# Performance work log

Hardware: AMD Instinct MI355X
Metric: run time of the kernel (lower is better)

## Reference

```python
import jax, jax.numpy as jnp
import numpy as np

HEADS = 16
DIM_HEAD = 64
SCALE = DIM_HEAD ** -0.5
EPS = 1e-5


def layer_norm(x, gamma):
    mu = jnp.mean(x, axis=-1, keepdims=True)
    var = jnp.var(x, axis=-1, keepdims=True)
    return (x - mu) * jax.lax.rsqrt(var + EPS) * gamma


def setup_inputs() -> dict:
    key = jax.random.key(0)
    ks = jax.random.split(key, 5)
    B, S, D = 2, 2048, 1024
    x = jax.random.normal(ks[0], (B, S, D), dtype=jnp.float32)
    gamma = jnp.ones((D,), dtype=jnp.float32)
    Wq = jax.random.normal(ks[1], (D, HEADS * DIM_HEAD), dtype=jnp.float32) * (D ** -0.5)
    Wkv = jax.random.normal(ks[2], (D, 2 * DIM_HEAD), dtype=jnp.float32) * (D ** -0.5)
    Wo = jax.random.normal(ks[3], (HEADS * DIM_HEAD, D), dtype=jnp.float32) * ((HEADS * DIM_HEAD) ** -0.5)
    return {"x": x, "gamma": gamma, "Wq": Wq, "Wkv": Wkv, "Wo": Wo}


def reference(x, gamma, Wq, Wkv, Wo):
    B, S, D = x.shape
    kv_input = x  # context=None -> self attention
    xn = layer_norm(x, gamma)
    q = xn @ Wq                          # [B,S,H*Dh]
    kv = kv_input @ Wkv                  # [B,S,2*Dh]
    k, v = jnp.split(kv, 2, axis=-1)     # each [B,S,Dh]
    q = q.reshape(B, S, HEADS, DIM_HEAD).transpose(0, 2, 1, 3) * SCALE  # [B,H,S,Dh]
    sim = jnp.einsum('bhid,bjd->bhij', q, k)  # [B,H,S,S]
    # causal mask: triu(j - i + 1) masked
    i_idx = jnp.arange(S)[:, None]
    j_idx = jnp.arange(S)[None, :]
    neg = -jnp.finfo(sim.dtype).max
    sim = jnp.where(j_idx > i_idx, neg, sim)
    attn = jax.nn.softmax(sim, axis=-1)
    out = jnp.einsum('bhij,bjd->bhid', attn, v)  # [B,H,S,Dh]
    out = out.transpose(0, 2, 1, 3).reshape(B, S, HEADS * DIM_HEAD)
    return out @ Wo
```

## Files before the change

kernel.cpp:

```cpp
#include <hip/hip_runtime.h>

typedef unsigned short u16;
typedef __attribute__((ext_vector_type(8))) u16    u16x8;
typedef __attribute__((ext_vector_type(4))) u16    u16x4;
typedef __attribute__((ext_vector_type(2))) unsigned u32x2;
typedef __attribute__((ext_vector_type(8))) __bf16 bf16x8;
typedef __attribute__((ext_vector_type(4))) float  f32x4;
typedef __attribute__((ext_vector_type(16))) float f32x16;

__device__ __forceinline__ u16 f2bf(float f) {
    unsigned u = __float_as_uint(f);
    u += 0x7fffu + ((u >> 16) & 1u);
    return (u16)(u >> 16);
}
__device__ __forceinline__ bf16x8 ldbf8(const u16* p) {
    return __builtin_bit_cast(bf16x8, *(const u16x8*)p);
}
__device__ __forceinline__ f32x4 mfma16(bf16x8 a, bf16x8 b, f32x4 c) {
    return __builtin_amdgcn_mfma_f32_16x16x32_bf16(a, b, c, 0, 0, 0);
}
__device__ __forceinline__ f32x16 mfma32x(bf16x8 a, bf16x8 b, f32x16 c) {
    return __builtin_amdgcn_mfma_f32_32x32x16_bf16(a, b, c, 0, 0, 0);
}
__device__ __forceinline__ float exp2a(float x) {
    float r; asm("v_exp_f32 %0, %1" : "=v"(r) : "v"(x)); return r;
}
__device__ __forceinline__ unsigned cvtpk(float lo, float hiv) {
    unsigned r; asm("v_cvt_pk_bf16_f32 %0, %1, %2" : "=v"(r) : "v"(lo), "v"(hiv)); return r;
}
__device__ __forceinline__ u32x2 permswap2(unsigned a, unsigned b) {
    return __builtin_amdgcn_permlane32_swap(a, b, false, false);
}
__device__ __forceinline__ float combine_sum(float x) {
    u32x2 pr = permswap2(__float_as_uint(x), __float_as_uint(x));
    return __uint_as_float(pr[0]) + __uint_as_float(pr[1]);
}
__device__ __forceinline__ bf16x8 pack4(unsigned a, unsigned b, unsigned c, unsigned d) {
    union { unsigned u[4]; bf16x8 v; } t; t.u[0] = a; t.u[1] = b; t.u[2] = c; t.u[3] = d; return t.v;
}

__global__ __launch_bounds__(256) void prep_kernel(const float* __restrict__ x, const float* __restrict__ gamma,
                                                   const float* __restrict__ Wq, const float* __restrict__ Wkv,
                                                   const float* __restrict__ Wo, u16* __restrict__ xn,
                                                   u16* __restrict__ xb, u16* __restrict__ Wq_t,
                                                   u16* __restrict__ Wkv_t, u16* __restrict__ Wo_t, float qscale) {
    const int bid = blockIdx.x, tid = threadIdx.x;
    if (bid < 4096) {
        const int row = bid;
        const float4 v = ((const float4*)(x + (size_t)row * 1024))[tid];
        float s  = v.x + v.y + v.z + v.w;
        float s2 = v.x * v.x + v.y * v.y + v.z * v.z + v.w * v.w;
#pragma unroll
        for (int off = 32; off; off >>= 1) { s += __shfl_down(s, off); s2 += __shfl_down(s2, off); }
        __shared__ float red[2][4];
        const int w = tid >> 6, lane = tid & 63;
        if (lane == 0) { red[0][w] = s; red[1][w] = s2; }
        __syncthreads();
        s  = red[0][0] + red[0][1] + red[0][2] + red[0][3];
        s2 = red[1][0] + red[1][1] + red[1][2] + red[1][3];
        const float mu  = s * (1.0f / 1024.0f);
        const float var = s2 * (1.0f / 1024.0f) - mu * mu;
        const float rs  = rsqrtf(var + 1e-5f);
        const float4 g = ((const float4*)gamma)[tid];
        u16x4 on, ob;
        on.x = f2bf((v.x - mu) * rs * g.x); on.y = f2bf((v.y - mu) * rs * g.y);
        on.z = f2bf((v.z - mu) * rs * g.z); on.w = f2bf((v.w - mu) * rs * g.w);
        ob.x = f2bf(v.x); ob.y = f2bf(v.y); ob.z = f2bf(v.z); ob.w = f2bf(v.w);
        ((u16x4*)(xn + (size_t)row * 1024))[tid] = on;
        ((u16x4*)(xb + (size_t)row * 1024))[tid] = ob;
    } else {
        __shared__ float tile[32][33];
        int bt = bid - 4096;
        int by = bt >> 5;
        const float* W; u16* Wt; int N; float scale;
        if (by < 32)      { W = Wq;  Wt = Wq_t;  N = 1024; scale = qscale; }
        else if (by < 36) { W = Wkv; Wt = Wkv_t; N = 128;  by -= 32; scale = 1.0f; }
        else              { W = Wo;  Wt = Wo_t;  N = 1024; by -= 36; scale = 1.0f; }
        const int K = 1024;
        const int kb = (bt & 31) * 32, nb = by * 32;
        const int tx = tid & 31, ty = tid >> 5;
#pragma unroll
        for (int i = 0; i < 32; i += 8)
            tile[ty + i][tx] = W[(size_t)(kb + ty + i) * N + nb + tx];
        __syncthreads();
#pragma unroll
        for (int i = 0; i < 32; i += 8)
            Wt[(size_t)(nb + ty + i) * K + kb + tx] = f2bf(tile[tx][ty + i] * scale);
    }
}

template<int EPI>
__device__ __forceinline__ void gemm_core(u16* lds, float (*kred)[128],
                                          const u16* __restrict__ A, const u16* __restrict__ Bt,
                                          u16* __restrict__ Cb, float* __restrict__ Cf, u16* __restrict__ Cv,
                                          int N, int K, int bx, int by, int tid) {
    constexpr int BM = 128, BN = 64, BK = 64;
    constexpr int WM = 64, WN = 32, FM = 4, FN = 2;
    constexpr int CPR = BK / 8, MS = CPR - 1;
    constexpr int CHA = BM * CPR, CH = (BM + BN) * CPR, ITERS = CH / 256;
    constexpr int LB = (BM + BN) * BK;
    const int m0 = bx * BM, n0 = by * BN;
    const int w = tid >> 6, lane = tid & 63, cl = lane & 15, kg = lane >> 4;
    const int wr = w >> 1, wc = w & 1;

    auto stage = [&](int buf, int k0) {
#pragma unroll
        for (int it = 0; it < ITERS; ++it) {
            int c = it * 256 + tid;
            const u16* g;
            if (c < CHA) { int r = c / CPR, cc = c & MS; g = A  + (size_t)(m0 + r) * K + k0 + ((cc ^ (r & MS)) * 8); }
            else { int c2 = c - CHA; int r = c2 / CPR, cc = c2 & MS; g = Bt + (size_t)(n0 + r) * K + k0 + ((cc ^ (r & MS)) * 8); }
            __builtin_amdgcn_global_load_lds(
                (const __attribute__((address_space(1))) unsigned int*)g,
                (__attribute__((address_space(3))) unsigned int*)&lds[buf * LB + c * 8], 16, 0, 0);
        }
    };

    const f32x4 zero = {0.f, 0.f, 0.f, 0.f};
    f32x4 acc[FM][FN];
#pragma unroll
    for (int m = 0; m < FM; m++)
#pragma unroll
        for (int n = 0; n < FN; n++) acc[m][n] = zero;

    const int KT = K / BK;
    stage(0, 0);
    for (int t = 0; t < KT; ++t) {
        __syncthreads();
        if (t + 1 < KT) stage((t + 1) & 1, (t + 1) * BK);
        const u16* As = &lds[(t & 1) * LB];
        const u16* Bs = &lds[(t & 1) * LB + BM * BK];
#pragma unroll
        for (int s = 0; s < BK / 32; s++) {
            bf16x8 af[FM], bfr[FN];
#pragma unroll
            for (int m = 0; m < FM; m++) {
                const int ra = wr * WM + m * 16 + cl;
                af[m] = ldbf8(As + ra * BK + (((s * 4 + kg) ^ (ra & MS)) * 8));
            }
#pragma unroll
            for (int n = 0; n < FN; n++) {
                const int rb = wc * WN + n * 16 + cl;
                bfr[n] = ldbf8(Bs + rb * BK + (((s * 4 + kg) ^ (rb & MS)) * 8));
            }
#pragma unroll
            for (int m = 0; m < FM; m++)
#pragma unroll
                for (int n = 0; n < FN; n++) acc[m][n] = mfma16(af[m], bfr[n], acc[m][n]);
        }
    }

#pragma unroll
    for (int m = 0; m < FM; m++)
#pragma unroll
        for (int n = 0; n < FN; n++)
#pragma unroll
            for (int r = 0; r < 4; r++) {
                const int row = m0 + wr * WM + m * 16 + kg * 4 + r;
                const int col = n0 + wc * WN + n * 16 + cl;
                const float v = acc[m][n][r];
                if constexpr (EPI == 0) Cb[(size_t)row * N + col] = f2bf(v);
                else if constexpr (EPI == 1) Cf[(size_t)row * N + col] = v;
                else {
                    if (col < 64) Cb[(size_t)row * 64 + col] = f2bf(v);
                    else { int bb = row >> 11, s = row & 2047;
                           Cv[((size_t)bb * 64 + (col - 64)) * 2048 + s] = f2bf(v); }
                }
            }

    if constexpr (EPI == 2) {
        if (n0 == 0) {
            float s2[FM][4];
#pragma unroll
            for (int m = 0; m < FM; m++)
#pragma unroll
                for (int r = 0; r < 4; r++) {
                    float t = 0.f;
#pragma unroll
                    for (int n = 0; n < FN; n++) {
                        const float vb = __uint_as_float(((unsigned)f2bf(acc[m][n][r])) << 16);
                        t = fmaf(vb, vb, t);
                    }
                    s2[m][r] = t;
                }
#pragma unroll
            for (int off = 1; off < 16; off <<= 1)
#pragma unroll
                for (int m = 0; m < FM; m++)
#pragma unroll
                    for (int r = 0; r < 4; r++) s2[m][r] += __shfl_xor(s2[m][r], off);
            if (cl == 0)
#pragma unroll
                for (int m = 0; m < FM; m++)
#pragma unroll
                    for (int r = 0; r < 4; r++) kred[wc][wr * 64 + m * 16 + kg * 4 + r] = s2[m][r];
            __syncthreads();
            if (tid < 64) {
                float t = fmaxf(kred[0][tid] + kred[1][tid], kred[0][tid + 64] + kred[1][tid + 64]);
#pragma unroll
                for (int off = 1; off < 64; off <<= 1) t = fmaxf(t, __shfl_xor(t, off));
                if (tid == 0) Cf[bx] = t;
            }
        }
    }
}

__global__ __launch_bounds__(256, 2) void gemm_qkv(const u16* __restrict__ xn, const u16* __restrict__ Wq_t,
                                                   u16* __restrict__ qb, const u16* __restrict__ xb,
                                                   const u16* __restrict__ Wkv_t, u16* __restrict__ kb,
                                                   u16* __restrict__ vtb, float* __restrict__ kpart) {
    __shared__ __align__(16) u16 lds[2 * 192 * 64];
    __shared__ float kred[2][128];
    const int tid = threadIdx.x;
    const int nwg = gridDim.x;
    int lin = blockIdx.x;
    lin = (lin & 7) * (nwg >> 3) + (lin >> 3);
    if (lin < 512) gemm_core<0>(lds, kred, xn, Wq_t, qb, nullptr, nullptr, 1024, 1024, lin & 31, lin >> 5, tid);
    else { int l2 = lin - 512; gemm_core<2>(lds, kred, xb, Wkv_t, kb, kpart, vtb, 128, 1024, l2 & 31, l2 >> 5, tid); }
}

__global__ __launch_bounds__(256, 2) void gemm_o(const u16* __restrict__ attb, const u16* __restrict__ Wo_t,
                                                 float* __restrict__ out) {
    __shared__ __align__(16) u16 lds[2 * 192 * 64];
    __shared__ float kred[2][128];
    const int tid = threadIdx.x;
    const int nwg = gridDim.x;
    int lin = blockIdx.x;
    lin = (lin & 7) * (nwg >> 3) + (lin >> 3);
    gemm_core<1>(lds, kred, attb, Wo_t, nullptr, out, nullptr, 1024, 1024, lin & 31, lin >> 5, tid);
}

__global__ __launch_bounds__(256, 2) void attn_fwd(const u16* __restrict__ q, const u16* __restrict__ k,
                                                   const u16* __restrict__ vt, const float* __restrict__ kpart,
                                                   u16* __restrict__ o) {
    constexpr int S = 2048;
    const int bid = blockIdx.x;
    const int p = (bid < 256) ? (bid >> 5) : (15 - ((bid - 256) >> 5));
    const int bh = bid & 31;
    const int h = bh & 15, b = bh >> 4;
    const int tid = threadIdx.x, w = tid >> 6, lane = tid & 63;
    const int pw = w & 1, par = w >> 1;
    const int l31 = lane & 31;
    const bool hi = (lane & 32) != 0;
    const int hi1 = hi ? 1 : 0, hi8 = hi ? 8 : 0;
    const int t1 = 2 * p + pw, t2 = 63 - t1;
    const int iters = 32 - p;
    const size_t bS = (size_t)b * S;

    __shared__ __align__(16) u16 smem[18432];

    auto stageK = [&](int jt, int buf, int tl) {
        const int r = tid >> 3, c = tid & 7;
        const u16* gp = k + (bS + jt * 32 + r) * 64 + ((c ^ (r & 7)) * 8);
        __builtin_amdgcn_global_load_lds(
            (const __attribute__((address_space(1))) unsigned int*)gp,
            (__attribute__((address_space(3))) unsigned int*)(smem + (buf * 2 + tl) * 2048 + tid * 8), 16, 0, 0);
    };
    auto loadV = [&](int jt) -> u16x8 {
        const int rv = tid >> 2, c4 = tid & 3;
        return *(const u16x8*)(vt + ((size_t)b * 64 + rv) * S + jt * 32 + c4 * 8);
    };
    auto writeV = [&](int buf, int tl, u16x8 v) {
        const int rv = tid >> 2, c4 = tid & 3;
        *(u16x8*)(smem + 8192 + (buf * 2 + tl) * 2560 + rv * 40 + c4 * 8) = v;
    };

    float km = kpart[(b << 4) + (l31 & 15)];
#pragma unroll
    for (int off = 1; off < 16; off <<= 1) km = fmaxf(km, __shfl_xor(km, off));
    const float kmaxb = sqrtf(km);

    bf16x8 qf1[4], qf2[4];
    float mB1, mB2;
    auto qload = [&](int t, bf16x8 (&qf)[4]) -> float {
        const u16* qp = q + (bS + t * 32 + l31) * 1024 + h * 64 + hi8;
        float qn2 = 0.f;
#pragma unroll
        for (int sub = 0; sub < 4; sub++) {
            qf[sub] = ldbf8(qp + sub * 16);
            const u16x8 uv = __builtin_bit_cast(u16x8, qf[sub]);
#pragma unroll
            for (int j = 0; j < 8; j++) {
                const float v = __uint_as_float(((unsigned)uv[j]) << 16);
                qn2 = fmaf(v, v, qn2);
            }
        }
        return sqrtf(combine_sum(qn2)) * kmaxb;
    };
    mB1 = qload(t1, qf1);
    mB2 = qload(t2, qf2);

    f32x16 a1lo, a1hi, a2lo, a2hi;
#pragma unroll
    for (int r = 0; r < 16; r++) { a1lo[r] = 0.f; a1hi[r] = 0.f; a2lo[r] = 0.f; a2hi[r] = 0.f; }
    float l1 = 0.f, l2 = 0.f;

    auto process = [&](const bf16x8 (&qf)[4], const bf16x8 (&kf)[4],
                       const bf16x8& vf00, const bf16x8& vf01, const bf16x8& vf10, const bf16x8& vf11,
                       f32x16& a0, f32x16& a1, float& lr, float mB, bool diag) {
        f32x16 s;
#pragma unroll
        for (int r = 0; r < 16; r++) s[r] = -mB;
#pragma unroll
        for (int sub = 0; sub < 4; sub++) s = mfma32x(kf[sub], qf[sub], s);
        if (diag) {
#pragma unroll
            for (int r = 0; r < 16; r++) {
                const int kvl = (r & 3) + 8 * (r >> 2) + (hi ? 4 : 0);
                if (kvl > l31) s[r] = -1e30f;
            }
        }
        float p0 = 0.f, p1 = 0.f;
#pragma unroll
        for (int r = 0; r < 16; r += 2) {
            const float ea = exp2a(s[r]);
            const float eb = exp2a(s[r + 1]);
            s[r] = ea; s[r + 1] = eb;
            p0 += ea; p1 += eb;
        }
        lr += p0 + p1;
        unsigned w0 = cvtpk(s[0], s[1]),  w1 = cvtpk(s[2], s[3]);
        unsigned w2 = cvtpk(s[4], s[5]),  w3 = cvtpk(s[6], s[7]);
        u32x2 r02 = permswap2(w0, w2), r13 = permswap2(w1, w3);
        bf16x8 pf0 = pack4(r02[0], r13[0], r02[1], r13[1]);
        unsigned y0 = cvtpk(s[8], s[9]),   y1 = cvtpk(s[10], s[11]);
        unsigned y2 = cvtpk(s[12], s[13]), y3 = cvtpk(s[14], s[15]);
        u32x2 t02 = permswap2(y0, y2), t13 = permswap2(y1, y3);
        bf16x8 pf1 = pack4(t02[0], t13[0], t02[1], t13[1]);
        a0 = mfma32x(vf00, pf0, a0);
        a0 = mfma32x(vf01, pf1, a0);
        a1 = mfma32x(vf10, pf0, a1);
        a1 = mfma32x(vf11, pf1, a1);
    };

    stageK(0, 0, 0); stageK(1, 0, 1);
    u16x8 v0 = loadV(0), v1 = loadV(1);
    for (int i = 0; i < iters; i++) {
        const int buf = i & 1;
        writeV(buf, 0, v0); writeV(buf, 1, v1);
        __syncthreads();
        if (i + 1 < iters) {
            stageK(2 * i + 2, buf ^ 1, 0); stageK(2 * i + 3, buf ^ 1, 1);
            v0 = loadV(2 * i + 2); v1 = loadV(2 * i + 3);
        }
        const int jt = 2 * i + par;
        if (jt <= t2) {
            const u16* kcur = smem + (buf * 2 + par) * 2048;
            const u16* vcur = smem + 8192 + (buf * 2 + par) * 2560;
            bf16x8 kf[4];
#pragma unroll
            for (int sub = 0; sub < 4; sub++)
                kf[sub] = ldbf8(kcur + l31 * 64 + (((sub * 2 + hi1) ^ (l31 & 7)) * 8));
            const bf16x8 vf00 = ldbf8(vcur + l31 * 40 + hi8);
            const bf16x8 vf01 = ldbf8(vcur + l31 * 40 + 16 + hi8);
            const bf16x8 vf10 = ldbf8(vcur + (32 + l31) * 40 + hi8);
            const bf16x8 vf11 = ldbf8(vcur + (32 + l31) * 40 + 16 + hi8);
            if (jt <= t1) process(qf1, kf, vf00, vf01, vf10, vf11, a1lo, a1hi, l1, mB1, jt == t1);
            process(qf2, kf, vf00, vf01, vf10, vf11, a2lo, a2hi, l2, mB2, jt == t2);
        }
    }
    float l1t = combine_sum(l1), l2t = combine_sum(l2);

    float* fm = (float*)smem;
    __syncthreads();
    {
        float* dst = fm + (((pw * 2) + (par ? 0 : 1)) * 64 + lane) * 36;
        if (par) { *(f32x16*)dst = a1lo; *(f32x16*)(dst + 16) = a1hi; dst[32] = l1t; }
        else     { *(f32x16*)dst = a2lo; *(f32x16*)(dst + 16) = a2hi; dst[32] = l2t; }
    }
    __syncthreads();
    {
        const float* src = fm + (((pw * 2) + (par ? 1 : 0)) * 64 + lane) * 36;
        const f32x16 s0 = *(const f32x16*)src;
        const f32x16 s1 = *(const f32x16*)(src + 16);
        if (par) {
#pragma unroll
            for (int r = 0; r < 16; r++) { a2lo[r] += s0[r]; a2hi[r] += s1[r]; }
            l2t += src[32];
        } else {
#pragma unroll
            for (int r = 0; r < 16; r++) { a1lo[r] += s0[r]; a1hi[r] += s1[r]; }
            l1t += src[32];
        }
    }
    __syncthreads();

    auto epi = [&](const f32x16& a0, const f32x16& a1, float lt, int t) {
        const float rl = 1.0f / lt;
        u16* lb = smem + w * 2304;
#pragma unroll
        for (int i = 0; i < 8; i++) {
            const int d = ((2 * i) & 3) + 8 * ((2 * i) >> 2) + (hi ? 4 : 0);
            *(unsigned*)&lb[l31 * 72 + d]      = cvtpk(a0[2 * i] * rl, a0[2 * i + 1] * rl);
            *(unsigned*)&lb[l31 * 72 + 32 + d] = cvtpk(a1[2 * i] * rl, a1[2 * i + 1] * rl);
        }
        asm volatile("s_waitcnt lgkmcnt(0)" ::: "memory");
#pragma unroll
        for (int i = 0; i < 4; i++) {
            const int qq = i * 8 + (lane >> 3), dd = (lane & 7) * 8;
            *(u16x8*)(o + (bS + t * 32 + qq) * 1024 + h * 64 + dd) = *(const u16x8*)&lb[qq * 72 + dd];
        }
    };
    if (par == 0) epi(a1lo, a1hi, l1t, t1);
    else          epi(a2lo, a2hi, l2t, t2);
}

extern "C" void kernel_launch(void* const* d_in, const int* in_sizes, int n_in,
                              void* d_out, int out_size, void* d_ws, size_t ws_size,
                              hipStream_t stream) {
    const float* x     = (const float*)d_in[0];
    const float* gamma = (const float*)d_in[1];
    const float* Wq    = (const float*)d_in[2];
    const float* Wkv   = (const float*)d_in[3];
    const float* Wo    = (const float*)d_in[4];
    float* out = (float*)d_out;
    char* ws = (char*)d_ws;

    u16* Wq_t  = (u16*)(ws + 0);
    u16* Wo_t  = (u16*)(ws + (2u << 20));
    u16* Wkv_t = (u16*)(ws + (4u << 20));
    u16* xn    = (u16*)(ws + 4456448u);
    u16* xb    = (u16*)(ws + 12845056u);
    u16* qb    = (u16*)(ws + 21233664u);
    u16* kb    = (u16*)(ws + 29622272u);
    u16* vtb   = (u16*)(ws + 30146560u);
    u16* attb  = (u16*)(ws + 30670848u);
    float* kpart = (float*)(ws + 39059456u);

    const float qscale = 0.125f * 1.44269504f;
    prep_kernel<<<4096 + 2176, 256, 0, stream>>>(x, gamma, Wq, Wkv, Wo, xn, xb, Wq_t, Wkv_t, Wo_t, qscale);
    gemm_qkv<<<576, 256, 0, stream>>>(xn, Wq_t, qb, xb, Wkv_t, kb, vtb, kpart);
    attn_fwd<<<512, 256, 0, stream>>>(qb, kb, vtb, kpart, attb);
    gemm_o<<<512, 256, 0, stream>>>(attb, Wo_t, out);
}
```

Baseline: 79.47 us.

## Stage four KV tiles per barrier and process two tiles per wave pair

The attention loop now stages four 32-row K/V tiles per iteration instead of two, so each wave parity handles two consecutive KV tiles between barriers. This halves the number of __syncthreads per block and lets K/V fragment loads sit inside process, next to their MFMAs. The V LDS row stride changes from 40 to 36, and the final reduction and epilogue are restructured so the par==0 waves write both query tiles. In exchange, LDS use roughly doubles to about 68KB per block, which may limit occupancy at 2 blocks per CU, and tail loads are guarded by kvmax.

Result: slower. 88.16 us (+10.9%).

```diff
diff --git a/kernel.cpp b/kernel.cpp
--- a/kernel.cpp
+++ b/kernel.cpp
@@ -244,25 +244,26 @@
     const bool hi = (lane & 32) != 0;
     const int hi1 = hi ? 1 : 0, hi8 = hi ? 8 : 0;
     const int t1 = 2 * p + pw, t2 = 63 - t1;
-    const int iters = 32 - p;
+    const int kvmax = 63 - 2 * p;
+    const int iters = (67 - 2 * p) >> 2;
     const size_t bS = (size_t)b * S;
 
-    __shared__ __align__(16) u16 smem[18432];
-
-    auto stageK = [&](int jt, int buf, int tl) {
+    __shared__ __align__(16) u16 smem[34816];
+
+    auto stageK = [&](int jt, int buf, int g) {
         const int r = tid >> 3, c = tid & 7;
         const u16* gp = k + (bS + jt * 32 + r) * 64 + ((c ^ (r & 7)) * 8);
         __builtin_amdgcn_global_load_lds(
             (const __attribute__((address_space(1))) unsigned int*)gp,
-            (__attribute__((address_space(3))) unsigned int*)(smem + (buf * 2 + tl) * 2048 + tid * 8), 16, 0, 0);
+            (__attribute__((address_space(3))) unsigned int*)(smem + buf * 17408 + g * 2048 + tid * 8), 16, 0, 0);
     };
     auto loadV = [&](int jt) -> u16x8 {
         const int rv = tid >> 2, c4 = tid & 3;
         return *(const u16x8*)(vt + ((size_t)b * 64 + rv) * S + jt * 32 + c4 * 8);
     };
-    auto writeV = [&](int buf, int tl, u16x8 v) {
+    auto writeV = [&](int buf, int g, u16x8 v) {
         const int rv = tid >> 2, c4 = tid & 3;
-        *(u16x8*)(smem + 8192 + (buf * 2 + tl) * 2560 + rv * 40 + c4 * 8) = v;
+        *(u16x8*)(smem + buf * 17408 + 8192 + g * 2304 + rv * 36 + c4 * 8) = v;
     };
 
     float km = kpart[(b << 4) + (l31 & 15)];
@@ -295,14 +296,21 @@
     for (int r = 0; r < 16; r++) { a1lo[r] = 0.f; a1hi[r] = 0.f; a2lo[r] = 0.f; a2hi[r] = 0.f; }
     float l1 = 0.f, l2 = 0.f;
 
-    auto process = [&](const bf16x8 (&qf)[4], const bf16x8 (&kf)[4],
-                       const bf16x8& vf00, const bf16x8& vf01, const bf16x8& vf10, const bf16x8& vf11,
+    auto process = [&](const bf16x8 (&qf)[4], const u16* kcur, const u16* vcur,
                        f32x16& a0, f32x16& a1, float& lr, float mB, bool diag) {
+        bf16x8 kf[4];
+#pragma unroll
+        for (int sub = 0; sub < 4; sub++)
+            kf[sub] = ldbf8(kcur + l31 * 64 + (((sub * 2 + hi1) ^ (l31 & 7)) * 8));
         f32x16 s;
 #pragma unroll
         for (int r = 0; r < 16; r++) s[r] = -mB;
 #pragma unroll
         for (int sub = 0; sub < 4; sub++) s = mfma32x(kf[sub], qf[sub], s);
+        const bf16x8 vf00 = ldbf8(vcur + l31 * 36 + hi8);
+        const bf16x8 vf01 = ldbf8(vcur + l31 * 36 + 16 + hi8);
+        const bf16x8 vf10 = ldbf8(vcur + (32 + l31) * 36 + hi8);
+        const bf16x8 vf11 = ldbf8(vcur + (32 + l31) * 36 + 16 + hi8);
         if (diag) {
 #pragma unroll
             for (int r = 0; r < 16; r++) {
@@ -333,76 +341,75 @@
         a1 = mfma32x(vf11, pf1, a1);
     };
 
-    stageK(0, 0, 0); stageK(1, 0, 1);
-    u16x8 v0 = loadV(0), v1 = loadV(1);
+    u16x8 v0 = loadV(0), v1 = loadV(1), v2 = loadV(2), v3 = loadV(3);
+    stageK(0, 0, 0); stageK(1, 0, 1); stageK(2, 0, 2); stageK(3, 0, 3);
     for (int i = 0; i < iters; i++) {
         const int buf = i & 1;
-        writeV(buf, 0, v0); writeV(buf, 1, v1);
+        writeV(buf, 0, v0); writeV(buf, 1, v1); writeV(buf, 2, v2); writeV(buf, 3, v3);
         __syncthreads();
         if (i + 1 < iters) {
-            stageK(2 * i + 2, buf ^ 1, 0); stageK(2 * i + 3, buf ^ 1, 1);
-            v0 = loadV(2 * i + 2); v1 = loadV(2 * i + 3);
-        }
-        const int jt = 2 * i + par;
-        if (jt <= t2) {
-            const u16* kcur = smem + (buf * 2 + par) * 2048;
-            const u16* vcur = smem + 8192 + (buf * 2 + par) * 2560;
-            bf16x8 kf[4];
-#pragma unroll
-            for (int sub = 0; sub < 4; sub++)
-                kf[sub] = ldbf8(kcur + l31 * 64 + (((sub * 2 + hi1) ^ (l31 & 7)) * 8));
-            const bf16x8 vf00 = ldbf8(vcur + l31 * 40 + hi8);
-            const bf16x8 vf01 = ldbf8(vcur + l31 * 40 + 16 + hi8);
-            const bf16x8 vf10 = ldbf8(vcur + (32 + l31) * 40 + hi8);
-            const bf16x8 vf11 = ldbf8(vcur + (32 + l31) * 40 + 16 + hi8);
-            if (jt <= t1) process(qf1, kf, vf00, vf01, vf10, vf11, a1lo, a1hi, l1, mB1, jt == t1);
-            process(qf2, kf, vf00, vf01, vf10, vf11, a2lo, a2hi, l2, mB2, jt == t2);
+            const int j0 = 4 * (i + 1);
+            if (j0 <= kvmax)     { stageK(j0, buf ^ 1, 0);     v0 = loadV(j0); }
+            if (j0 + 1 <= kvmax) { stageK(j0 + 1, buf ^ 1, 1); v1 = loadV(j0 + 1); }
+            if (j0 + 2 <= kvmax) { stageK(j0 + 2, buf ^ 1, 2); v2 = loadV(j0 + 2); }
+            if (j0 + 3 <= kvmax) { stageK(j0 + 3, buf ^ 1, 3); v3 = loadV(j0 + 3); }
+        }
+        const int jt0 = 4 * i + 2 * par, jt1 = jt0 + 1;
+        const int g0 = 2 * par, g1 = g0 + 1;
+        const u16* kc0 = smem + buf * 17408 + g0 * 2048;
+        const u16* vc0 = smem + buf * 17408 + 8192 + g0 * 2304;
+        const u16* kc1 = smem + buf * 17408 + g1 * 2048;
+        const u16* vc1 = smem + buf * 17408 + 8192 + g1 * 2304;
+        if (jt0 <= t2) {
+            if (jt0 <= t1) process(qf1, kc0, vc0, a1lo, a1hi, l1, mB1, jt0 == t1);
+            process(qf2, kc0, vc0, a2lo, a2hi, l2, mB2, jt0 == t2);
+        }
+        if (jt1 <= t2) {
+            if (jt1 <= t1) process(qf1, kc1, vc1, a1lo, a1hi, l1, mB1, jt1 == t1);
+            process(qf2, kc1, vc1, a2lo, a2hi, l2, mB2, jt1 == t2);
         }
     }
     float l1t = combine_sum(l1), l2t = combine_sum(l2);
 
     float* fm = (float*)smem;
     __syncthreads();
-    {
-        float* dst = fm + (((pw * 2) + (par ? 0 : 1)) * 64 + lane) * 36;
-        if (par) { *(f32x16*)dst = a1lo; *(f32x16*)(dst + 16) = a1hi; dst[32] = l1t; }
-        else     { *(f32x16*)dst = a2lo; *(f32x16*)(dst + 16) = a2hi; dst[32] = l2t; }
+    if (par == 1) {
+        float* d = fm + ((size_t)(pw * 64) + lane) * 68;
+        *(f32x16*)d        = a1lo; *(f32x16*)(d + 16) = a1hi;
+        *(f32x16*)(d + 32) = a2lo; *(f32x16*)(d + 48) = a2hi;
+        d[64] = l1t; d[65] = l2t;
     }
     __syncthreads();
-    {
-        const float* src = fm + (((pw * 2) + (par ? 1 : 0)) * 64 + lane) * 36;
-        const f32x16 s0 = *(const f32x16*)src;
-        const f32x16 s1 = *(const f32x16*)(src + 16);
-        if (par) {
-#pragma unroll
-            for (int r = 0; r < 16; r++) { a2lo[r] += s0[r]; a2hi[r] += s1[r]; }
-            l2t += src[32];
-        } else {
-#pragma unroll
-            for (int r = 0; r < 16; r++) { a1lo[r] += s0[r]; a1hi[r] += s1[r]; }
-            l1t += src[32];
-        }
+    if (par == 0) {
+        const float* sp = fm + ((size_t)(pw * 64) + lane) * 68;
+        const f32x16 b0 = *(const f32x16*)sp,        b1 = *(const f32x16*)(sp + 16);
+        const f32x16 b2 = *(const f32x16*)(sp + 32), b3 = *(const f32x16*)(sp + 48);
+#pragma unroll
+        for (int r = 0; r < 16; r++) { a1lo[r] += b0[r]; a1hi[r] += b1[r]; a2lo[r] += b2[r]; a2hi[r] += b3[r]; }
+        l1t += sp[64]; l2t += sp[65];
     }
     __syncthreads();
 
-    auto epi = [&](const f32x16& a0, const f32x16& a1, float lt, int t) {
-        const float rl = 1.0f / lt;
-        u16* lb = smem + w * 2304;
-#pragma unroll
-        for (int i = 0; i < 8; i++) {
-            const int d = ((2 * i) & 3) + 8 * ((2 * i) >> 2) + (hi ? 4 : 0);
-            *(unsigned*)&lb[l31 * 72 + d]      = cvtpk(a0[2 * i] * rl, a0[2 * i + 1] * rl);
-            *(unsigned*)&lb[l31 * 72 + 32 + d] = cvtpk(a1[2 * i] * rl, a1[2 * i + 1] * rl);
-        }
-        asm volatile("s_waitcnt lgkmcnt(0)" ::: "memory");
-#pragma unroll
-        for (int i = 0; i < 4; i++) {
-            const int qq = i * 8 + (lane >> 3), dd = (lane & 7) * 8;
-            *(u16x8*)(o + (bS + t * 32 + qq) * 1024 + h * 64 + dd) = *(const u16x8*)&lb[qq * 72 + dd];
-        }
-    };
-    if (par == 0) epi(a1lo, a1hi, l1t, t1);
-    else          epi(a2lo, a2hi, l2t, t2);
+    if (par == 0) {
+        auto epi = [&](const f32x16& a0, const f32x16& a1, float lt, int t, int which) {
+            const float rl = 1.0f / lt;
+            u16* lb = smem + (pw * 2 + which) * 2304;
+#pragma unroll
+            for (int i = 0; i < 8; i++) {
+                const int d = ((2 * i) & 3) + 8 * ((2 * i) >> 2) + (hi ? 4 : 0);
+                *(unsigned*)&lb[l31 * 72 + d]      = cvtpk(a0[2 * i] * rl, a0[2 * i + 1] * rl);
+                *(unsigned*)&lb[l31 * 72 + 32 + d] = cvtpk(a1[2 * i] * rl, a1[2 * i + 1] * rl);
+            }
+            asm volatile("s_waitcnt lgkmcnt(0)" ::: "memory");
+#pragma unroll
+            for (int i = 0; i < 4; i++) {
+                const int qq = i * 8 + (lane >> 3), dd = (lane & 7) * 8;
+                *(u16x8*)(o + (bS + t * 32 + qq) * 1024 + h * 64 + dd) = *(const u16x8*)&lb[qq * 72 + dd];
+            }
+        };
+        epi(a1lo, a1hi, l1t, t1, 0);
+        epi(a2lo, a2hi, l2t, t2, 1);
+    }
 }
 
 extern "C" void kernel_launch(void* const* d_in, const int* in_sizes, int n_in,
```
